# Optimization experiments

Hardware: AMD Instinct MI355X
Metric: run time of the kernel (lower is better)

The kernel has to match this reference:

```python
import jax, jax.numpy as jnp
import numpy as np

DT = 1e-3
TMIN = 0.0


def setup_inputs() -> dict:
    key = jax.random.key(0)
    k_fd, k_w1, k_w2, k_n = jax.random.split(key, 4)
    batch, steps, length, hidden = 512, 500, 128, 512
    forward_diffusion = jax.random.normal(k_fd, (batch, steps, length), dtype=jnp.float32)
    W1 = jax.random.normal(k_w1, (length + 1, hidden), dtype=jnp.float32) * 0.02
    b1 = jnp.zeros((hidden,), dtype=jnp.float32)
    W2 = jax.random.normal(k_w2, (hidden, length), dtype=jnp.float32) * 0.02
    b2 = jnp.zeros((length,), dtype=jnp.float32)
    noise = jax.random.normal(k_n, (steps - 1, length), dtype=jnp.float32)
    return {"forward_diffusion": forward_diffusion, "W1": W1, "b1": b1,
            "W2": W2, "b2": b2, "noise": noise}


def reference(forward_diffusion, W1, b1, W2, b2, noise):
    # forward_diffusion: (batch, steps, length); noise: (steps-1, length)
    steps = noise.shape[0] + 1
    time = TMIN + DT * jnp.arange(steps, dtype=jnp.float32)
    sqrt_dt = jnp.sqrt(jnp.float32(DT))
    x0 = forward_diffusion[:, -1, :]                       # (batch, length)
    batch = x0.shape[0]

    def score(x, t):
        bt = jnp.full((batch, 1), t, dtype=x.dtype)        # tf.repeat of t
        inp = jnp.concatenate([x, bt], axis=1)             # (batch, length+1)
        h = jax.nn.relu(inp @ W1 + b1)
        return h @ W2 + b2                                 # (batch, length)

    def body(x, inp):
        t, eps = inp
        mu = -0.5 * x                                      # mu(x, t)
        sig = jnp.float32(1.0)                             # sigma(x, t)
        x_new = x + (mu - sig * sig * score(x, t)) * DT + sig * sqrt_dt * eps
        return x_new, x_new

    # loop runs step = steps-1 down to 1
    ts = time[1:][::-1]                                    # (steps-1,)
    _, ys = jax.lax.scan(body, x0, (ts, noise))            # ys: (steps-1, batch, length)
    # TensorArray index 0 holds x0; index k (k>=1) holds the state written at step k,
    # which is the (steps-k)-th scan output -> out[1:] = flip(ys)
    out = jnp.concatenate([x0[None], ys[::-1]], axis=0)    # (steps, batch, length)
    return jnp.transpose(out, (1, 0, 2))                   # (batch, steps, length)
```

## Files before the change

kernel.cpp:

```cpp
#include <hip/hip_runtime.h>
#include <stdint.h>

typedef float f32x4 __attribute__((ext_vector_type(4)));
typedef short s16x8 __attribute__((ext_vector_type(8)));
typedef short s16x4 __attribute__((ext_vector_type(4)));
typedef unsigned int u32;

#define NSTEPS 499
#define LEN    128
#define HID    512
#define TROW   64000

union frag8 { s16x8 v; u32 u[4]; };
union fvec4 { f32x4 v; float f[4]; };

#define PIN_FRAG(fr) asm volatile("" : "+v"((fr).u[0]), "+v"((fr).u[1]), \
                                       "+v"((fr).u[2]), "+v"((fr).u[3]))
#define PIN_F4(fv)   asm volatile("" : "+v"((fv).f[0]), "+v"((fv).f[1]), \
                                       "+v"((fv).f[2]), "+v"((fv).f[3]))

__device__ __forceinline__ short f2bf_rne(float f) {
  union { float f; u32 u; } v; v.f = f;
  u32 r = (v.u + 0x7FFFu + ((v.u >> 16) & 1u)) >> 16;
  return (short)(r & 0xFFFFu);
}

__device__ __forceinline__ s16x4 pack4(f32x4 v) {
  union { float f; u32 u; } c0, c1, c2, c3;
  c0.f = v[0]; c1.f = v[1]; c2.f = v[2]; c3.f = v[3];
  u32 u0 = c0.u + 0x8000u, u1 = c1.u + 0x8000u;
  u32 u2 = c2.u + 0x8000u, u3 = c3.u + 0x8000u;
  union { u32 x[2]; s16x4 s; } r;
  r.x[0] = __builtin_amdgcn_perm(u1, u0, 0x07060302u);
  r.x[1] = __builtin_amdgcn_perm(u3, u2, 0x07060302u);
  return r.s;
}

__global__ __launch_bounds__(512, 2)
void cond_diff_kernel(const float* __restrict__ fd,
                      const float* __restrict__ W1,
                      const float* __restrict__ b1,
                      const float* __restrict__ W2,
                      const float* __restrict__ b2,
                      const float* __restrict__ noise,
                      float* __restrict__ out)
{
  const int tid  = threadIdx.x;
  const int w    = tid >> 6;
  const int lane = tid & 63;
  const int q    = lane >> 4;
  const int lc   = lane & 15;
  const int bb   = blockIdx.x << 4;

  __shared__ short xbf[16 * 16 * 8];
  __shared__ short hbf[64 * 16 * 8];

  frag8 a1[4][4];
#pragma unroll
  for (int t = 0; t < 4; ++t) {
    const int j = 64 * w + 16 * t + lc;
#pragma unroll
    for (int s = 0; s < 4; ++s) {
      s16x8 f;
#pragma unroll
      for (int i = 0; i < 8; ++i)
        f[i] = f2bf_rne(W1[(32 * s + 8 * q + i) * HID + j]);
      a1[t][s].v = f;
      PIN_FRAG(a1[t][s]);
    }
  }
  frag8 a2[16];
#pragma unroll
  for (int s = 0; s < 16; ++s) {
    const int kb = 32 * s + 8 * q;
    s16x8 f;
#pragma unroll
    for (int i = 0; i < 8; ++i)
      f[i] = f2bf_rne(W2[(kb + i) * LEN + 16 * w + lc]);
    a2[s].v = f;
    PIN_FRAG(a2[s]);
  }

  fvec4 bb1[4], bw1[4];
#pragma unroll
  for (int t = 0; t < 4; ++t) {
    const int j0 = 64 * w + 16 * t + 4 * q;
    bb1[t].v = *(const f32x4*)(b1 + j0);
    bw1[t].v = *(const f32x4*)(W1 + 128 * HID + j0);
    PIN_F4(bb1[t]); PIN_F4(bw1[t]);
  }
  const int l0 = 16 * w + 4 * q;
  fvec4 nb2;
  {
    f32x4 b2v = *(const f32x4*)(b2 + l0);
#pragma unroll
    for (int r = 0; r < 4; ++r) nb2.f[r] = -0.001f * b2v[r];
    PIN_F4(nb2);
  }

  const int obase = (bb + lc) * TROW;
  f32x4 xm = *(const f32x4*)(fd + obase + NSTEPS * LEN + l0);
  *(f32x4*)(out + obase + l0) = xm;
  *(s16x4*)(&xbf[((l0 >> 3) * 16 + lc) * 8 + (l0 & 7)]) = pack4(xm);
  __syncthreads();

  const float DTc = 0.001f;
  const float SD  = 0.031622776601683794f;
  const float C0  = 0.9995f;

#pragma unroll 1
  for (int k = 0; k < NSTEPS; ++k) {
    const float tt = DTc * (float)(NSTEPS - k);

    f32x4 eps = *(const f32x4*)(noise + k * LEN + l0);

    f32x4 acc1[4];
#pragma unroll
    for (int t = 0; t < 4; ++t)
#pragma unroll
      for (int r = 0; r < 4; ++r)
        acc1[t][r] = __builtin_fmaf(tt, bw1[t].f[r], bb1[t].f[r]);
#pragma unroll
    for (int s = 0; s < 4; ++s) {
      const s16x8 bf = *(const s16x8*)(&xbf[((4 * s + q) * 16 + lc) * 8]);
#pragma unroll
      for (int t = 0; t < 4; ++t)
        acc1[t] = __builtin_amdgcn_mfma_f32_16x16x32_bf16(a1[t][s].v, bf, acc1[t], 0, 0, 0);
    }
#pragma unroll
    for (int t = 0; t < 4; ++t) {
      f32x4 h;
#pragma unroll
      for (int r = 0; r < 4; ++r) h[r] = fmaxf(acc1[t][r], 0.f);
      const int jb = 64 * w + 16 * t + 4 * q;
      *(s16x4*)(&hbf[((jb >> 3) * 16 + lc) * 8 + (jb & 7)]) = pack4(h);
    }
    __syncthreads();

    f32x4 acc2[4];
#pragma unroll
    for (int c = 0; c < 4; ++c) acc2[c] = (f32x4){0.f, 0.f, 0.f, 0.f};
#pragma unroll
    for (int i = 0; i < 4; ++i) {
#pragma unroll
      for (int c = 0; c < 4; ++c) {
        const int s = 4 * c + i;
        const s16x8 bf = *(const s16x8*)(&hbf[((4 * s + q) * 16 + lc) * 8]);
        acc2[c] = __builtin_amdgcn_mfma_f32_16x16x32_bf16(a2[s].v, bf, acc2[c], 0, 0, 0);
      }
    }

    f32x4 xn;
#pragma unroll
    for (int r = 0; r < 4; ++r) {
      const float sc = (acc2[0][r] + acc2[1][r]) + (acc2[2][r] + acc2[3][r]);
      const float t1 = __builtin_fmaf(SD, eps[r], nb2.f[r]);
      const float t2 = __builtin_fmaf(-DTc, sc, t1);
      xn[r] = __builtin_fmaf(C0, xm[r], t2);
    }
    xm = xn;
    *(s16x4*)(&xbf[((l0 >> 3) * 16 + lc) * 8 + (l0 & 7)]) = pack4(xn);
    __syncthreads();

    *(f32x4*)(out + obase + (NSTEPS - k) * LEN + l0) = xn;
  }
}

extern "C" void kernel_launch(void* const* d_in, const int* in_sizes, int n_in,
                              void* d_out, int out_size, void* d_ws, size_t ws_size,
                              hipStream_t stream) {
  const float* fd    = (const float*)d_in[0];
  const float* W1    = (const float*)d_in[1];
  const float* b1    = (const float*)d_in[2];
  const float* W2    = (const float*)d_in[3];
  const float* b2    = (const float*)d_in[4];
  const float* noise = (const float*)d_in[5];
  (void)in_sizes; (void)n_in; (void)out_size; (void)d_ws; (void)ws_size;
  cond_diff_kernel<<<dim3(32), dim3(512), 0, stream>>>(fd, W1, b1, W2, b2, noise,
                                                       (float*)d_out);
}
```

Baseline: 694.2 us.

## Halve block to four waves, each computing twice the hidden and output tiles

Shrinks each block from 8 to 4 wavefronts. Each wave now holds twice as many W1 and W2 bf16 fragments in registers and computes 8 hidden tiles and 2 output column tiles per step. This is meant to cut the cost of the two __syncthreads per step, since fewer waves take part in each barrier, and to give the MFMA chains more independent work per wave. In exchange it raises register pressure substantially (more pinned fragments) and has fewer waves available to hide latency on the serial per-step critical path.

```diff
diff --git a/kernel.cpp b/kernel.cpp
--- a/kernel.cpp
+++ b/kernel.cpp
@@ -36,7 +36,7 @@
   return r.s;
 }
 
-__global__ __launch_bounds__(512, 2)
+__global__ __launch_bounds__(256, 1)
 void cond_diff_kernel(const float* __restrict__ fd,
                       const float* __restrict__ W1,
                       const float* __restrict__ b1,
@@ -55,10 +55,10 @@
   __shared__ short xbf[16 * 16 * 8];
   __shared__ short hbf[64 * 16 * 8];
 
-  frag8 a1[4][4];
+  frag8 a1[8][4];
 #pragma unroll
-  for (int t = 0; t < 4; ++t) {
-    const int j = 64 * w + 16 * t + lc;
+  for (int t = 0; t < 8; ++t) {
+    const int j = 128 * w + 16 * t + lc;
 #pragma unroll
     for (int s = 0; s < 4; ++s) {
       s16x8 f;
@@ -69,39 +69,47 @@
       PIN_FRAG(a1[t][s]);
     }
   }
-  frag8 a2[16];
+  frag8 a2[2][16];
 #pragma unroll
-  for (int s = 0; s < 16; ++s) {
-    const int kb = 32 * s + 8 * q;
-    s16x8 f;
+  for (int p = 0; p < 2; ++p) {
 #pragma unroll
-    for (int i = 0; i < 8; ++i)
-      f[i] = f2bf_rne(W2[(kb + i) * LEN + 16 * w + lc]);
-    a2[s].v = f;
-    PIN_FRAG(a2[s]);
+    for (int s = 0; s < 16; ++s) {
+      const int kb = 32 * s + 8 * q;
+      s16x8 f;
+#pragma unroll
+      for (int i = 0; i < 8; ++i)
+        f[i] = f2bf_rne(W2[(kb + i) * LEN + 16 * (2 * w + p) + lc]);
+      a2[p][s].v = f;
+      PIN_FRAG(a2[p][s]);
+    }
   }
 
-  fvec4 bb1[4], bw1[4];
+  fvec4 bb1[8], bw1[8];
 #pragma unroll
-  for (int t = 0; t < 4; ++t) {
-    const int j0 = 64 * w + 16 * t + 4 * q;
+  for (int t = 0; t < 8; ++t) {
+    const int j0 = 128 * w + 16 * t + 4 * q;
     bb1[t].v = *(const f32x4*)(b1 + j0);
     bw1[t].v = *(const f32x4*)(W1 + 128 * HID + j0);
     PIN_F4(bb1[t]); PIN_F4(bw1[t]);
   }
-  const int l0 = 16 * w + 4 * q;
-  fvec4 nb2;
+  const int l0a = 32 * w + 4 * q;
+  const int l0b = l0a + 16;
+  fvec4 nb2[2];
   {
-    f32x4 b2v = *(const f32x4*)(b2 + l0);
+    f32x4 va = *(const f32x4*)(b2 + l0a);
+    f32x4 vb = *(const f32x4*)(b2 + l0b);
 #pragma unroll
-    for (int r = 0; r < 4; ++r) nb2.f[r] = -0.001f * b2v[r];
-    PIN_F4(nb2);
+    for (int r = 0; r < 4; ++r) { nb2[0].f[r] = -0.001f * va[r]; nb2[1].f[r] = -0.001f * vb[r]; }
+    PIN_F4(nb2[0]); PIN_F4(nb2[1]);
   }
 
   const int obase = (bb + lc) * TROW;
-  f32x4 xm = *(const f32x4*)(fd + obase + NSTEPS * LEN + l0);
-  *(f32x4*)(out + obase + l0) = xm;
-  *(s16x4*)(&xbf[((l0 >> 3) * 16 + lc) * 8 + (l0 & 7)]) = pack4(xm);
+  f32x4 xmA = *(const f32x4*)(fd + obase + NSTEPS * LEN + l0a);
+  f32x4 xmB = *(const f32x4*)(fd + obase + NSTEPS * LEN + l0b);
+  *(f32x4*)(out + obase + l0a) = xmA;
+  *(f32x4*)(out + obase + l0b) = xmB;
+  *(s16x4*)(&xbf[((l0a >> 3) * 16 + lc) * 8 + (l0a & 7)]) = pack4(xmA);
+  *(s16x4*)(&xbf[((l0b >> 3) * 16 + lc) * 8 + (l0b & 7)]) = pack4(xmB);
   __syncthreads();
 
   const float DTc = 0.001f;
@@ -112,11 +120,12 @@
   for (int k = 0; k < NSTEPS; ++k) {
     const float tt = DTc * (float)(NSTEPS - k);
 
-    f32x4 eps = *(const f32x4*)(noise + k * LEN + l0);
+    f32x4 epsA = *(const f32x4*)(noise + k * LEN + l0a);
+    f32x4 epsB = *(const f32x4*)(noise + k * LEN + l0b);
 
-    f32x4 acc1[4];
+    f32x4 acc1[8];
 #pragma unroll
-    for (int t = 0; t < 4; ++t)
+    for (int t = 0; t < 8; ++t)
 #pragma unroll
       for (int r = 0; r < 4; ++r)
         acc1[t][r] = __builtin_fmaf(tt, bw1[t].f[r], bb1[t].f[r]);
@@ -124,45 +133,51 @@
     for (int s = 0; s < 4; ++s) {
       const s16x8 bf = *(const s16x8*)(&xbf[((4 * s + q) * 16 + lc) * 8]);
 #pragma unroll
-      for (int t = 0; t < 4; ++t)
+      for (int t = 0; t < 8; ++t)
         acc1[t] = __builtin_amdgcn_mfma_f32_16x16x32_bf16(a1[t][s].v, bf, acc1[t], 0, 0, 0);
     }
 #pragma unroll
-    for (int t = 0; t < 4; ++t) {
+    for (int t = 0; t < 8; ++t) {
       f32x4 h;
 #pragma unroll
       for (int r = 0; r < 4; ++r) h[r] = fmaxf(acc1[t][r], 0.f);
-      const int jb = 64 * w + 16 * t + 4 * q;
+      const int jb = 128 * w + 16 * t + 4 * q;
       *(s16x4*)(&hbf[((jb >> 3) * 16 + lc) * 8 + (jb & 7)]) = pack4(h);
     }
     __syncthreads();
 
-    f32x4 acc2[4];
+    f32x4 acc2[2][2];
 #pragma unroll
-    for (int c = 0; c < 4; ++c) acc2[c] = (f32x4){0.f, 0.f, 0.f, 0.f};
+    for (int p = 0; p < 2; ++p)
 #pragma unroll
-    for (int i = 0; i < 4; ++i) {
+      for (int c = 0; c < 2; ++c) acc2[p][c] = (f32x4){0.f, 0.f, 0.f, 0.f};
 #pragma unroll
-      for (int c = 0; c < 4; ++c) {
-        const int s = 4 * c + i;
-        const s16x8 bf = *(const s16x8*)(&hbf[((4 * s + q) * 16 + lc) * 8]);
-        acc2[c] = __builtin_amdgcn_mfma_f32_16x16x32_bf16(a2[s].v, bf, acc2[c], 0, 0, 0);
-      }
+    for (int s = 0; s < 16; ++s) {
+      const s16x8 bf = *(const s16x8*)(&hbf[((4 * s + q) * 16 + lc) * 8]);
+      acc2[0][s & 1] = __builtin_amdgcn_mfma_f32_16x16x32_bf16(a2[0][s].v, bf, acc2[0][s & 1], 0, 0, 0);
+      acc2[1][s & 1] = __builtin_amdgcn_mfma_f32_16x16x32_bf16(a2[1][s].v, bf, acc2[1][s & 1], 0, 0, 0);
     }
 
-    f32x4 xn;
+    f32x4 xnA, xnB;
 #pragma unroll
     for (int r = 0; r < 4; ++r) {
-      const float sc = (acc2[0][r] + acc2[1][r]) + (acc2[2][r] + acc2[3][r]);
-      const float t1 = __builtin_fmaf(SD, eps[r], nb2.f[r]);
-      const float t2 = __builtin_fmaf(-DTc, sc, t1);
-      xn[r] = __builtin_fmaf(C0, xm[r], t2);
+      const float scA = acc2[0][0][r] + acc2[0][1][r];
+      const float t1A = __builtin_fmaf(SD, epsA[r], nb2[0].f[r]);
+      const float t2A = __builtin_fmaf(-DTc, scA, t1A);
+      xnA[r] = __builtin_fmaf(C0, xmA[r], t2A);
+      const float scB = acc2[1][0][r] + acc2[1][1][r];
+      const float t1B = __builtin_fmaf(SD, epsB[r], nb2[1].f[r]);
+      const float t2B = __builtin_fmaf(-DTc, scB, t1B);
+      xnB[r] = __builtin_fmaf(C0, xmB[r], t2B);
     }
-    xm = xn;
-    *(s16x4*)(&xbf[((l0 >> 3) * 16 + lc) * 8 + (l0 & 7)]) = pack4(xn);
+    xmA = xnA; xmB = xnB;
+    *(s16x4*)(&xbf[((l0a >> 3) * 16 + lc) * 8 + (l0a & 7)]) = pack4(xnA);
+    *(s16x4*)(&xbf[((l0b >> 3) * 16 + lc) * 8 + (l0b & 7)]) = pack4(xnB);
     __syncthreads();
 
-    *(f32x4*)(out + obase + (NSTEPS - k) * LEN + l0) = xn;
+    const int orow = obase + (NSTEPS - k) * LEN;
+    *(f32x4*)(out + orow + l0a) = xnA;
+    *(f32x4*)(out + orow + l0b) = xnB;
   }
 }
 
@@ -176,6 +191,6 @@
   const float* b2    = (const float*)d_in[4];
   const float* noise = (const float*)d_in[5];
   (void)in_sizes; (void)n_in; (void)out_size; (void)d_ws; (void)ws_size;
-  cond_diff_kernel<<<dim3(32), dim3(512), 0, stream>>>(fd, W1, b1, W2, b2, noise,
+  cond_diff_kernel<<<dim3(32), dim3(256), 0, stream>>>(fd, W1, b1, W2, b2, noise,
                                                        (float*)d_out);
 }
```

Result: slower. 1.081 ms (+55.7%).

## Use scaled FP8 MFMA for second layer with repacked hidden activations in LDS

Applied to the files above, without the earlier changes.

The second matmul (hidden to score) now uses fp8 weights and fp8 hidden activations with the 16x16x32 fp8 MFMA instead of bf16. W1/b1 are prescaled by 32 and W2 by 64 so the values sit in a usable fp8 range, and the result is rescaled by 1/2048. The LDS layout for the hidden activations is changed so each lane reads two k-slices with one 16-byte load, halving LDS traffic and W2 register footprint. This trades accuracy for less work per step, and rounding error can accumulate over the 499-step recurrence.

```diff
diff --git a/kernel.cpp b/kernel.cpp
--- a/kernel.cpp
+++ b/kernel.cpp
@@ -2,9 +2,11 @@
 #include <stdint.h>
 
 typedef float f32x4 __attribute__((ext_vector_type(4)));
+typedef int   i32x4 __attribute__((ext_vector_type(4)));
 typedef short s16x8 __attribute__((ext_vector_type(8)));
 typedef short s16x4 __attribute__((ext_vector_type(4)));
 typedef unsigned int u32;
+typedef long i64;
 
 #define NSTEPS 499
 #define LEN    128
@@ -12,12 +14,14 @@
 #define TROW   64000
 
 union frag8 { s16x8 v; u32 u[4]; };
+union fragq { i64 l; u32 u[2]; };
 union fvec4 { f32x4 v; float f[4]; };
 
-#define PIN_FRAG(fr) asm volatile("" : "+v"((fr).u[0]), "+v"((fr).u[1]), \
-                                       "+v"((fr).u[2]), "+v"((fr).u[3]))
-#define PIN_F4(fv)   asm volatile("" : "+v"((fv).f[0]), "+v"((fv).f[1]), \
-                                       "+v"((fv).f[2]), "+v"((fv).f[3]))
+#define PIN_FRAG(fr)  asm volatile("" : "+v"((fr).u[0]), "+v"((fr).u[1]), \
+                                        "+v"((fr).u[2]), "+v"((fr).u[3]))
+#define PIN_FRAGQ(fr) asm volatile("" : "+v"((fr).u[0]), "+v"((fr).u[1]))
+#define PIN_F4(fv)    asm volatile("" : "+v"((fv).f[0]), "+v"((fv).f[1]), \
+                                        "+v"((fv).f[2]), "+v"((fv).f[3]))
 
 __device__ __forceinline__ short f2bf_rne(float f) {
   union { float f; u32 u; } v; v.f = f;
@@ -34,6 +38,11 @@
   r.x[0] = __builtin_amdgcn_perm(u1, u0, 0x07060302u);
   r.x[1] = __builtin_amdgcn_perm(u3, u2, 0x07060302u);
   return r.s;
+}
+
+template <bool HI>
+__device__ __forceinline__ u32 cvt2_fp8(float a, float b, u32 old) {
+  return (u32)__builtin_amdgcn_cvt_pk_fp8_f32(a, b, (int)old, HI);
 }
 
 __global__ __launch_bounds__(512, 2)
@@ -53,7 +62,8 @@
   const int bb   = blockIdx.x << 4;
 
   __shared__ short xbf[16 * 16 * 8];
-  __shared__ short hbf[64 * 16 * 8];
+  __shared__ i32x4 hq4[512];
+  unsigned char* const hqp = (unsigned char*)hq4;
 
   frag8 a1[4][4];
 #pragma unroll
@@ -64,29 +74,32 @@
       s16x8 f;
 #pragma unroll
       for (int i = 0; i < 8; ++i)
-        f[i] = f2bf_rne(W1[(32 * s + 8 * q + i) * HID + j]);
+        f[i] = f2bf_rne(32.0f * W1[(32 * s + 8 * q + i) * HID + j]);
       a1[t][s].v = f;
       PIN_FRAG(a1[t][s]);
     }
   }
-  frag8 a2[16];
+  fragq a2[16];
 #pragma unroll
   for (int s = 0; s < 16; ++s) {
     const int kb = 32 * s + 8 * q;
-    s16x8 f;
-#pragma unroll
-    for (int i = 0; i < 8; ++i)
-      f[i] = f2bf_rne(W2[(kb + i) * LEN + 16 * w + lc]);
-    a2[s].v = f;
-    PIN_FRAG(a2[s]);
+    const float* wp = W2 + 16 * w + lc;
+    u32 u0 = cvt2_fp8<false>(64.f * wp[(kb + 0) * LEN], 64.f * wp[(kb + 1) * LEN], 0u);
+    u0     = cvt2_fp8<true >(64.f * wp[(kb + 2) * LEN], 64.f * wp[(kb + 3) * LEN], u0);
+    u32 u1 = cvt2_fp8<false>(64.f * wp[(kb + 4) * LEN], 64.f * wp[(kb + 5) * LEN], 0u);
+    u1     = cvt2_fp8<true >(64.f * wp[(kb + 6) * LEN], 64.f * wp[(kb + 7) * LEN], u1);
+    a2[s].u[0] = u0; a2[s].u[1] = u1;
+    PIN_FRAGQ(a2[s]);
   }
 
   fvec4 bb1[4], bw1[4];
 #pragma unroll
   for (int t = 0; t < 4; ++t) {
     const int j0 = 64 * w + 16 * t + 4 * q;
-    bb1[t].v = *(const f32x4*)(b1 + j0);
-    bw1[t].v = *(const f32x4*)(W1 + 128 * HID + j0);
+    f32x4 b1v = *(const f32x4*)(b1 + j0);
+    f32x4 w1t = *(const f32x4*)(W1 + 128 * HID + j0);
+#pragma unroll
+    for (int r = 0; r < 4; ++r) { bb1[t].f[r] = 32.f * b1v[r]; bw1[t].f[r] = 32.f * w1t[r]; }
     PIN_F4(bb1[t]); PIN_F4(bw1[t]);
   }
   const int l0 = 16 * w + 4 * q;
@@ -107,6 +120,7 @@
   const float DTc = 0.001f;
   const float SD  = 0.031622776601683794f;
   const float C0  = 0.9995f;
+  const float NS  = -0.001f / 2048.0f;
 
 #pragma unroll 1
   for (int k = 0; k < NSTEPS; ++k) {
@@ -132,8 +146,11 @@
       f32x4 h;
 #pragma unroll
       for (int r = 0; r < 4; ++r) h[r] = fmaxf(acc1[t][r], 0.f);
-      const int jb = 64 * w + 16 * t + 4 * q;
-      *(s16x4*)(&hbf[((jb >> 3) * 16 + lc) * 8 + (jb & 7)]) = pack4(h);
+      u32 hw = cvt2_fp8<false>(h[0], h[1], 0u);
+      hw     = cvt2_fp8<true >(h[2], h[3], hw);
+      const int kk = 16 * t + 4 * q;
+      *(u32*)(hqp + w * 1024 + (((kk >> 3) & 3) * 16 + lc) * 16
+                  + ((kk >> 5) * 8) + (kk & 7)) = hw;
     }
     __syncthreads();
 
@@ -141,13 +158,15 @@
 #pragma unroll
     for (int c = 0; c < 4; ++c) acc2[c] = (f32x4){0.f, 0.f, 0.f, 0.f};
 #pragma unroll
-    for (int i = 0; i < 4; ++i) {
-#pragma unroll
-      for (int c = 0; c < 4; ++c) {
-        const int s = 4 * c + i;
-        const s16x8 bf = *(const s16x8*)(&hbf[((4 * s + q) * 16 + lc) * 8]);
-        acc2[c] = __builtin_amdgcn_mfma_f32_16x16x32_bf16(a2[s].v, bf, acc2[c], 0, 0, 0);
-      }
+    for (int g = 0; g < 8; ++g) {
+      const i32x4 rv = *(const i32x4*)(hqp + g * 1024 + (q * 16 + lc) * 16);
+      fragq lo, hi;
+      lo.u[0] = rv[0]; lo.u[1] = rv[1];
+      hi.u[0] = rv[2]; hi.u[1] = rv[3];
+      acc2[(2 * g) & 3]     = __builtin_amdgcn_mfma_f32_16x16x32_fp8_fp8(
+                                a2[2 * g].l, lo.l, acc2[(2 * g) & 3], 0, 0, 0);
+      acc2[(2 * g + 1) & 3] = __builtin_amdgcn_mfma_f32_16x16x32_fp8_fp8(
+                                a2[2 * g + 1].l, hi.l, acc2[(2 * g + 1) & 3], 0, 0, 0);
     }
 
     f32x4 xn;
@@ -155,7 +174,7 @@
     for (int r = 0; r < 4; ++r) {
       const float sc = (acc2[0][r] + acc2[1][r]) + (acc2[2][r] + acc2[3][r]);
       const float t1 = __builtin_fmaf(SD, eps[r], nb2.f[r]);
-      const float t2 = __builtin_fmaf(-DTc, sc, t1);
+      const float t2 = __builtin_fmaf(NS, sc, t1);
       xn[r] = __builtin_fmaf(C0, xm[r], t2);
     }
     xm = xn;
```

After: 648.0 us. 1.07x faster.
